# Kernel optimization log

Measured on AMD Instinct MI355X. Metric: run time of the kernel, lower is better.

## Reference

```python
import jax, jax.numpy as jnp
import numpy as np

B, S, D = 16, 4096, 64
N_HASHES = 8
BUCKET_SIZE = 64
N_BUCKETS = S // BUCKET_SIZE  # 64
NEG = -5e4  # the module uses -50000.0 as masking value
EPS = 1e-6


def setup_inputs() -> dict:
    key = jax.random.key(0)
    k1, k2, k3 = jax.random.split(key, 3)
    qk = jax.random.normal(k1, (B, S, D), dtype=jnp.float32)
    v = jax.random.normal(k2, (B, S, D), dtype=jnp.float32)
    # random rotations for LSH: (batch, dim, n_hashes, n_buckets//2)
    rotations = jax.random.normal(k3, (B, D, N_HASHES, N_BUCKETS // 2), dtype=jnp.float32)
    return {"qk": qk, "v": v, "rotations": rotations, "seed_": 0}


def _look_one_back(x):
    # prepend previous chunk (with wraparound) along the key axis
    x_extra = jnp.concatenate([x[:, -1:], x[:, :-1]], axis=1)
    return jnp.concatenate([x, x_extra], axis=2)


def reference(qk, v, rotations, seed_):
    b, s, d = qk.shape
    n_hashes = rotations.shape[2]
    n_buckets = 2 * rotations.shape[3]
    chunks = n_hashes * n_buckets  # n_bins == n_buckets

    # ---- hash_vectors ----
    rot = jnp.einsum('btf,bfhi->bhti', qk, rotations)          # (b, h, s, nb/2)
    rot = jnp.concatenate([rot, -rot], axis=-1)                # (b, h, s, nb)
    buckets = jnp.argmax(rot, axis=-1)                         # (b, h, s)
    offsets = (jnp.arange(n_hashes) * n_buckets)[None, :, None]
    buckets = (buckets + offsets).reshape(b, n_hashes * s)     # (b, h*s)

    # ---- sort by (bucket, position) ----
    ticker = jnp.arange(n_hashes * s)
    buckets_and_t = s * buckets + (ticker % s)[None, :]
    sticker = jnp.argsort(buckets_and_t, axis=-1)              # stable sort indices
    undo_sort = jnp.argsort(sticker, axis=-1)

    st = sticker % s                                           # original positions
    sqk = jnp.take_along_axis(qk, st[..., None], axis=1)       # (b, h*s, d)
    sv = jnp.take_along_axis(v, st[..., None], axis=1)

    bq_t = st.reshape(b, chunks, -1)                           # (b, chunks, bucket)
    bqk = sqk.reshape(b, chunks, -1, d)
    bv = sv.reshape(b, chunks, -1, d)

    bq = bqk
    norm = jnp.linalg.norm(bqk, axis=-1, keepdims=True)
    bk = bqk / (norm + EPS)                                    # make_unit_length

    bk = _look_one_back(bk)                                    # (b, chunks, 2*bucket, d)
    bv = _look_one_back(bv)
    bkv_t = _look_one_back(bq_t[..., None])[..., 0]            # (b, chunks, 2*bucket)

    dots = jnp.einsum('bhie,bhje->bhij', bq, bk) * (d ** -0.5)
    self_mask = bq_t[:, :, :, None] == bkv_t[:, :, None, :]
    dots = jnp.where(self_mask, NEG, dots)

    dots_lse = jax.nn.logsumexp(dots, axis=-1, keepdims=True)  # (b, chunks, bucket, 1)
    probs = jnp.exp(dots - dots_lse)
    bo = jnp.einsum('buij,buje->buie', probs, bv)              # (b, chunks, bucket, d)

    so = bo.reshape(b, n_hashes * s, d)
    slogits = dots_lse.reshape(b, n_hashes * s)

    # ---- unsort ----
    o = jnp.take_along_axis(so, undo_sort[..., None], axis=1)
    logits = jnp.take_along_axis(slogits, undo_sort, axis=-1)

    # ---- combine hash rounds via logsumexp weights ----
    o = o.reshape(b, n_hashes, s, d)
    logits = logits.reshape(b, n_hashes, s, 1)
    w = jnp.exp(logits - jax.nn.logsumexp(logits, axis=1, keepdims=True))
    out = jnp.sum(o * w, axis=1)                               # (b, s, d)
    return out, buckets
```

## Files before the change

### kernel.cpp

```cpp
#include <hip/hip_runtime.h>
#include <math.h>

#define BB   16
#define SS   4096
#define DD   64
#define HH   8
#define NBH  32
#define NB   64
#define NCH  512

typedef __attribute__((ext_vector_type(8))) short s16x8;
typedef __attribute__((ext_vector_type(4))) short s16x4;
typedef __attribute__((ext_vector_type(4))) float f32x4;

static __device__ __forceinline__ unsigned short f2bf(float x) {
  union { float f; unsigned u; } a; a.f = x;
  unsigned r = a.u + 0x7fffu + ((a.u >> 16) & 1u);
  return (unsigned short)(r >> 16);
}
static __device__ __forceinline__ float bf2f(unsigned short u) {
  union { unsigned u; float f; } a; a.u = ((unsigned)u) << 16;
  return a.f;
}

__global__ __launch_bounds__(256) void k_conv(
    const float* __restrict__ qk, const float* __restrict__ v,
    unsigned short* __restrict__ qb, unsigned short* __restrict__ kb,
    unsigned short* __restrict__ vb) {
  const int gid = blockIdx.x * 256 + threadIdx.x;
  const int half = BB * SS * 4;
  const bool isV = gid >= half;
  const int id = isV ? gid - half : gid;
  const int row = id >> 2, q4 = id & 3;

  const float4* src =
      (const float4*)((isV ? v : qk) + (size_t)row * DD + q4 * 16);
  float vals[16];
#pragma unroll
  for (int g = 0; g < 4; g++) {
    const float4 a = src[g];
    vals[g * 4 + 0] = a.x; vals[g * 4 + 1] = a.y;
    vals[g * 4 + 2] = a.z; vals[g * 4 + 3] = a.w;
  }

  if (!isV) {
    float ss = 0.f;
#pragma unroll
    for (int i = 0; i < 16; i++) ss += vals[i] * vals[i];
    ss += __shfl_xor(ss, 1);
    ss += __shfl_xor(ss, 2);
    const float scl = 0.125f / (sqrtf(ss) + 1e-6f);
    unsigned short qo[16], ko[16];
#pragma unroll
    for (int i = 0; i < 16; i++) {
      qo[i] = f2bf(vals[i]);
      ko[i] = f2bf(vals[i] * scl);
    }
    unsigned short* qd = qb + (size_t)row * DD + q4 * 16;
    unsigned short* kd = kb + (size_t)row * DD + q4 * 16;
    *(s16x8*)qd = *(const s16x8*)&qo[0];
    *(s16x8*)(qd + 8) = *(const s16x8*)&qo[8];
    *(s16x8*)kd = *(const s16x8*)&ko[0];
    *(s16x8*)(kd + 8) = *(const s16x8*)&ko[8];
  } else {
    unsigned short vo[16];
#pragma unroll
    for (int i = 0; i < 16; i++) vo[i] = f2bf(vals[i]);
    unsigned short* vd = vb + (size_t)row * DD + q4 * 16;
    *(s16x8*)vd = *(const s16x8*)&vo[0];
    *(s16x8*)(vd + 8) = *(const s16x8*)&vo[8];
  }
}

__global__ __launch_bounds__(256) void k_rotT(
    const float* __restrict__ rot, unsigned short* __restrict__ rTh,
    unsigned short* __restrict__ rTl, int* __restrict__ needy_count) {
  __shared__ float slab[32][256];
  const int b = blockIdx.x;
  const int tid = threadIdx.x;
  if (b == 0 && tid == 0) *needy_count = 0;

  for (int st = 0; st < 2; st++) {
#pragma unroll
    for (int fr = 0; fr < 32; fr++)
      slab[fr][tid] = rot[(size_t)b * (DD * HH * NBH) +
                          (size_t)(st * 32 + fr) * 256 + tid];
    __syncthreads();
    unsigned short hi[32], lo[32];
#pragma unroll
    for (int fr = 0; fr < 32; fr++) {
      const float x = slab[fr][tid];
      const unsigned short hh = f2bf(x);
      hi[fr] = hh;
      lo[fr] = f2bf(x - bf2f(hh));
    }
    unsigned short* dh = rTh + ((size_t)b * 256 + tid) * DD + st * 32;
    unsigned short* dl = rTl + ((size_t)b * 256 + tid) * DD + st * 32;
#pragma unroll
    for (int g = 0; g < 4; g++) {
      *(s16x8*)(dh + g * 8) = *(const s16x8*)&hi[g * 8];
      *(s16x8*)(dl + g * 8) = *(const s16x8*)&lo[g * 8];
    }
    __syncthreads();
  }
}

#define MARGIN 1e-2f

__global__ __launch_bounds__(256, 2) void k_hash_mfma(
    const float* __restrict__ qk, const unsigned short* __restrict__ rTh,
    const unsigned short* __restrict__ rTl, int* __restrict__ bucket_local,
    float* __restrict__ buckets_out, int* __restrict__ needy_list,
    int* __restrict__ needy_count) {
  __shared__ struct __align__(16) {
    unsigned short ah[128][72];
    unsigned short al[128][72];
    float sc[128][33];
  } sm;
  const int b = blockIdx.x;
  const int t0 = blockIdx.y * 128;
  const int tid = threadIdx.x;
  const int w = tid >> 6, lane = tid & 63;
  const int quad = lane >> 4, l16 = lane & 15;

  {
    const int row = tid >> 1, hf = tid & 1;
    const float4* src =
        (const float4*)(qk + ((size_t)b * SS + t0 + row) * DD + hf * 32);
#pragma unroll
    for (int gg = 0; gg < 4; gg++) {
      const float4 v0 = src[gg * 2], v1 = src[gg * 2 + 1];
      const float a[8] = {v0.x, v0.y, v0.z, v0.w, v1.x, v1.y, v1.z, v1.w};
      unsigned short hi[8], lo[8];
#pragma unroll
      for (int e = 0; e < 8; e++) {
        const unsigned short hh = f2bf(a[e]);
        hi[e] = hh;
        lo[e] = f2bf(a[e] - bf2f(hh));
      }
      *(s16x8*)&sm.ah[row][hf * 32 + gg * 8] = *(const s16x8*)hi;
      *(s16x8*)&sm.al[row][hf * 32 + gg * 8] = *(const s16x8*)lo;
    }
  }
  __syncthreads();

  s16x8 Ah[2][2], Al[2][2];
#pragma unroll
  for (int mtl = 0; mtl < 2; mtl++) {
    const int row = (w * 2 + mtl) * 16 + l16;
#pragma unroll
    for (int ks = 0; ks < 2; ks++) {
      Ah[mtl][ks] = *(const s16x8*)&sm.ah[row][ks * 32 + quad * 8];
      Al[mtl][ks] = *(const s16x8*)&sm.al[row][ks * 32 + quad * 8];
    }
  }

#pragma unroll 1
  for (int h = 0; h < HH; h++) {
#pragma unroll
    for (int nt = 0; nt < 2; nt++) {
      const size_t rrow = (((size_t)b * HH + h) * 32 + nt * 16 + l16) * DD;
      s16x8 Bh2[2], Bl2[2];
#pragma unroll
      for (int ks = 0; ks < 2; ks++) {
        Bh2[ks] = *(const s16x8*)&rTh[rrow + ks * 32 + quad * 8];
        Bl2[ks] = *(const s16x8*)&rTl[rrow + ks * 32 + quad * 8];
      }
#pragma unroll
      for (int mtl = 0; mtl < 2; mtl++) {
        f32x4 acc = (f32x4){0.f, 0.f, 0.f, 0.f};
#pragma unroll
        for (int ks = 0; ks < 2; ks++) {
          acc = __builtin_amdgcn_mfma_f32_16x16x32_bf16(Al[mtl][ks], Bl2[ks], acc, 0, 0, 0);
          acc = __builtin_amdgcn_mfma_f32_16x16x32_bf16(Al[mtl][ks], Bh2[ks], acc, 0, 0, 0);
          acc = __builtin_amdgcn_mfma_f32_16x16x32_bf16(Ah[mtl][ks], Bl2[ks], acc, 0, 0, 0);
          acc = __builtin_amdgcn_mfma_f32_16x16x32_bf16(Ah[mtl][ks], Bh2[ks], acc, 0, 0, 0);
        }
#pragma unroll
        for (int r = 0; r < 4; r++)
          sm.sc[(w * 2 + mtl) * 16 + quad * 4 + r][nt * 16 + l16] = acc[r];
      }
    }
    __syncthreads();

    if (lane < 32) {
      const int tloc = w * 32 + lane;
      float best = -3.0e38f, second = -3.0e38f;
      int bi = 0;
#pragma unroll 8
      for (int i = 0; i < 32; i++) {
        const float vv = sm.sc[tloc][i];
        if (vv > best) { second = best; best = vv; bi = i; }
        else if (vv > second) second = vv;
      }
#pragma unroll 8
      for (int i = 32; i < 64; i++) {
        const float vv = -sm.sc[tloc][i - 32];
        if (vv > best) { second = best; best = vv; bi = i; }
        else if (vv > second) second = vv;
      }
      const int t = t0 + tloc;
      bucket_local[((size_t)b * HH + h) * SS + t] = bi;
      buckets_out[(size_t)b * (HH * SS) + (size_t)h * SS + t] =
          (float)(h * NB + bi);
      if (best - second <= MARGIN) {
        const int slot = atomicAdd(needy_count, 1);
        needy_list[slot] = (((b << 3) | h) << 12) | t;
      }
    }
    __syncthreads();
  }
}

__global__ __launch_bounds__(256) void k_hash_fix(
    const float* __restrict__ qk, const float* __restrict__ rot,
    const int* __restrict__ needy_list, const int* __restrict__ needy_count,
    int* __restrict__ bucket_local, float* __restrict__ buckets_out) {
  const int n = *needy_count;
  const int hw = (blockIdx.x * 256 + (int)threadIdx.x) >> 5;
  const int li = threadIdx.x & 31;
  const int nhw = gridDim.x * 8;

  for (int idx = hw; idx < n; idx += nhw) {
    const int code = needy_list[idx];
    const int t = code & 4095;
    const int bh = code >> 12;
    const int b = bh >> 3, h = bh & 7;

    const float* qrow = qk + ((size_t)b * SS + t) * DD;
    const float* rcol = rot + ((size_t)b * DD * HH + h) * NBH + li;

    double acc = 0.0;
#pragma unroll 8
    for (int f = 0; f < DD; f++)
      acc += (double)qrow[f] * (double)rcol[(size_t)f * (HH * NBH)];

    double bv = acc;
    int bi = li;
    if (-acc > bv) { bv = -acc; bi = li + 32; }
#pragma unroll
    for (int off = 1; off < 32; off <<= 1) {
      const double ov = __shfl_xor(bv, off);
      const int oi = __shfl_xor(bi, off);
      if (ov > bv || (ov == bv && oi < bi)) { bv = ov; bi = oi; }
    }
    if (li == 0) {
      bucket_local[((size_t)b * HH + h) * SS + t] = bi;
      buckets_out[(size_t)b * (HH * SS) + (size_t)h * SS + t] =
          (float)(h * NB + bi);
    }
  }
}

__global__ __launch_bounds__(256) void k_sort(
    const int* __restrict__ bucket_local, int* __restrict__ sort_t,
    int* __restrict__ ipos) {
  __shared__ unsigned short lb[SS];
  __shared__ unsigned char  cnt[NB][256];
  __shared__ unsigned short pfx[NB][256];
  __shared__ int part[NB][4];
  __shared__ int tot[NB];
  __shared__ int base[NB];

  const int bh = blockIdx.x;
  const int tid = threadIdx.x;
  const int* src = bucket_local + (size_t)bh * SS;

  int* czero = (int*)&cnt[0][0];
#pragma unroll
  for (int i = 0; i < 16; i++) czero[tid + i * 256] = 0;
  __syncthreads();

#pragma unroll
  for (int i = 0; i < 16; i++) {
    const int t = tid * 16 + i;
    const int v = src[t];
    lb[t] = (unsigned short)v;
    cnt[v][tid]++;
  }
  __syncthreads();

  {
    const int bk = tid & 63, sg = tid >> 6;
    int s = 0;
#pragma unroll 8
    for (int i = 0; i < 64; i++) s += cnt[bk][sg * 64 + i];
    part[bk][sg] = s;
  }
  __syncthreads();
  if (tid < NB) tot[tid] = part[tid][0] + part[tid][1] + part[tid][2] + part[tid][3];
  __syncthreads();
  if (tid == 0) {
    int r = 0;
    for (int i = 0; i < NB; i++) { base[i] = r; r += tot[i]; }
  }
  __syncthreads();
  {
    const int bk = tid & 63, sg = tid >> 6;
    int run = base[bk];
    for (int s = 0; s < sg; s++) run += part[bk][s];
#pragma unroll 8
    for (int i = 0; i < 64; i++) {
      const int th = sg * 64 + i;
      pfx[bk][th] = (unsigned short)run;
      run += cnt[bk][th];
    }
  }
  __syncthreads();
  int* st = sort_t + (size_t)bh * SS;
  int* ip = ipos + (size_t)bh * SS;
#pragma unroll
  for (int i = 0; i < 16; i++) {
    const int t = tid * 16 + i;
    const int bk = lb[t];
    const int pos = pfx[bk][tid]++;
    st[pos] = t;
    ip[t] = pos;
  }
}

__global__ __launch_bounds__(256, 4) void k_attn2(
    const unsigned short* __restrict__ qb, const unsigned short* __restrict__ kbg,
    const unsigned short* __restrict__ vbg, const int* __restrict__ sort_t,
    unsigned short* __restrict__ so, float* __restrict__ lse_u) {
  const int blk = blockIdx.x;
  const int b = blk >> 9;
  const int c = blk & 511;
  const int h = c >> 6, cc = c & 63;
  const int cp = (c + 511) & 511;
  const int hp = cp >> 6, ccp = cp & 63;

  __shared__ struct __align__(16) {
    union {
      unsigned short kb[128][72];
      unsigned short p[64][136];
    } kp;
    unsigned short vs[128][68];
    int tk[128];
  } sm;

  const int tid = threadIdx.x;
  const int w = tid >> 6;
  const int lane = tid & 63;
  const int quad = lane >> 4;
  const int l16 = lane & 15;

  if (tid < 128) {
    const size_t srci = (tid < 64)
        ? (((size_t)b * HH + h) * SS + cc * 64 + tid)
        : (((size_t)b * HH + hp) * SS + ccp * 64 + (tid - 64));
    sm.tk[tid] = sort_t[srci];
  }
  __syncthreads();

  {
    const int j = tid >> 1, hf = tid & 1;
    const int trow = sm.tk[j];
    const s16x8* ksrc = (const s16x8*)(kbg + ((size_t)b * SS + trow) * DD + hf * 32);
    const s16x8* vsrc = (const s16x8*)(vbg + ((size_t)b * SS + trow) * DD + hf * 32);
    s16x8 kr[4], vr[4];
#pragma unroll
    for (int g = 0; g < 4; g++) { kr[g] = ksrc[g]; vr[g] = vsrc[g]; }
#pragma unroll
    for (int g = 0; g < 4; g++)
      *(s16x8*)&sm.kp.kb[j][hf * 32 + g * 8] = kr[g];
#pragma unroll
    for (int g = 0; g < 4; g++) {
      *(s16x4*)&sm.vs[j][hf * 32 + g * 8] = (s16x4){vr[g][0], vr[g][1], vr[g][2], vr[g][3]};
      *(s16x4*)&sm.vs[j][hf * 32 + g * 8 + 4] = (s16x4){vr[g][4], vr[g][5], vr[g][6], vr[g][7]};
    }
  }
  const int tq_frag = sm.tk[w * 16 + l16];
  const unsigned short* qrowp = qb + ((size_t)b * SS + tq_frag) * DD;
  const s16x8 a0 = *(const s16x8*)(qrowp + quad * 8);
  const s16x8 a1 = *(const s16x8*)(qrowp + 32 + quad * 8);
  __syncthreads();

  f32x4 acc[8];
#pragma unroll
  for (int nt = 0; nt < 8; nt++) acc[nt] = (f32x4){0.f, 0.f, 0.f, 0.f};
#pragma unroll
  for (int nt = 0; nt < 8; nt++) {
    const s16x8 b0 = *(const s16x8*)&sm.kp.kb[nt * 16 + l16][quad * 8];
    const s16x8 b1 = *(const s16x8*)&sm.kp.kb[nt * 16 + l16][32 + quad * 8];
    acc[nt] = __builtin_amdgcn_mfma_f32_16x16x32_bf16(a0, b0, acc[nt], 0, 0, 0);
    acc[nt] = __builtin_amdgcn_mfma_f32_16x16x32_bf16(a1, b1, acc[nt], 0, 0, 0);
  }

  int tqr[4];
#pragma unroll
  for (int r = 0; r < 4; r++) tqr[r] = sm.tk[w * 16 + quad * 4 + r];
  int tkc[8];
#pragma unroll
  for (int nt = 0; nt < 8; nt++) tkc[nt] = sm.tk[nt * 16 + l16];

#pragma unroll
  for (int nt = 0; nt < 8; nt++)
#pragma unroll
    for (int r = 0; r < 4; r++)
      if (tqr[r] == tkc[nt]) acc[nt][r] = -50000.0f;

  float rmax[4], lse[4], inv[4];
#pragma unroll
  for (int r = 0; r < 4; r++) {
    float m = acc[0][r];
#pragma unroll
    for (int nt = 1; nt < 8; nt++) m = fmaxf(m, acc[nt][r]);
    m = fmaxf(m, __shfl_xor(m, 1));
    m = fmaxf(m, __shfl_xor(m, 2));
    m = fmaxf(m, __shfl_xor(m, 4));
    m = fmaxf(m, __shfl_xor(m, 8));
    rmax[r] = m;
  }
#pragma unroll
  for (int r = 0; r < 4; r++) {
    float s = 0.f;
#pragma unroll
    for (int nt = 0; nt < 8; nt++) {
      const float e = __expf(acc[nt][r] - rmax[r]);
      acc[nt][r] = e;
      s += e;
    }
    s += __shfl_xor(s, 1);
    s += __shfl_xor(s, 2);
    s += __shfl_xor(s, 4);
    s += __shfl_xor(s, 8);
    inv[r] = 1.0f / s;
    lse[r] = __logf(s) + rmax[r];
  }

  if (l16 == 0) {
#pragma unroll
    for (int r = 0; r < 4; r++)
      lse_u[((size_t)b * SS + tqr[r]) * HH + h] = lse[r];
  }

  __syncthreads();

#pragma unroll
  for (int nt = 0; nt < 8; nt++)
#pragma unroll
    for (int r = 0; r < 4; r++)
      sm.kp.p[w * 16 + quad * 4 + r][nt * 16 + l16] = f2bf(acc[nt][r] * inv[r]);
  __syncthreads();

  f32x4 o[4];
#pragma unroll
  for (int nt = 0; nt < 4; nt++) o[nt] = (f32x4){0.f, 0.f, 0.f, 0.f};
#pragma unroll
  for (int kc = 0; kc < 4; kc++) {
    s16x8 av;
#pragma unroll
    for (int e = 0; e < 8; e++)
      av[e] = (short)sm.vs[kc * 32 + quad * 8 + e][w * 16 + l16];
#pragma unroll
    for (int nt = 0; nt < 4; nt++) {
      const s16x8 bp = *(const s16x8*)&sm.kp.p[nt * 16 + l16][kc * 32 + quad * 8];
      o[nt] = __builtin_amdgcn_mfma_f32_16x16x32_bf16(av, bp, o[nt], 0, 0, 0);
    }
  }

#pragma unroll
  for (int nt = 0; nt < 4; nt++) {
    const int t = sm.tk[nt * 16 + l16];
    s16x4 ov;
#pragma unroll
    for (int r = 0; r < 4; r++) ov[r] = (short)f2bf(o[nt][r]);
    unsigned short* dst =
        so + (((size_t)b * SS + t) * HH + h) * DD + w * 16 + quad * 4;
    *(s16x4*)dst = ov;
  }
}

__global__ __launch_bounds__(256) void k_combine2(
    const unsigned short* __restrict__ so, const float* __restrict__ lse_u,
    float* __restrict__ out) {
  const size_t idx = (size_t)blockIdx.x * 256 + threadIdx.x;
  const int f = (int)(idx & 63);
  const size_t bt = idx >> 6;

  float l[HH];
#pragma unroll
  for (int h = 0; h < HH; h++) l[h] = lse_u[bt * HH + h];
  float m = l[0];
#pragma unroll
  for (int h = 1; h < HH; h++) m = fmaxf(m, l[h]);
  float den = 0.f, num = 0.f;
#pragma unroll
  for (int h = 0; h < HH; h++) {
    const float wgt = __expf(l[h] - m);
    den += wgt;
    num += wgt * bf2f(so[(bt * HH + h) * DD + f]);
  }
  out[idx] = num / den;
}

__global__ __launch_bounds__(256, 2) void k_hash_f32(
    const float* __restrict__ qk, const float* __restrict__ rot,
    int* __restrict__ bucket_local, float* __restrict__ buckets_out,
    int* __restrict__ needy_list, int* __restrict__ needy_count) {
  __shared__ float lb[128 * 65];
  const int b = blockIdx.x;
  const int t0 = blockIdx.y * 128;
  const int tid = threadIdx.x;

  {
    const int row = tid >> 1, hf = (tid & 1) * 32;
    const float4* src =
        (const float4*)(qk + ((size_t)b * SS + t0 + row) * DD + hf);
    float* dst = &lb[row * 65 + hf];
#pragma unroll
    for (int g = 0; g < 8; g++) {
      const float4 vv = src[g];
      dst[g * 4 + 0] = vv.x; dst[g * 4 + 1] = vv.y;
      dst[g * 4 + 2] = vv.z; dst[g * 4 + 3] = vv.w;
    }
  }
  __syncthreads();

  const int w = tid >> 6;
  const int l = tid & 63;
  const int hb = __builtin_amdgcn_readfirstlane(w);

  for (int hp = 0; hp < 2; hp++) {
    const int h = hb + hp * 4;
    const float* rbase = rot + ((size_t)b * DD * HH + h) * NBH;
    const size_t rstride = HH * NBH;

    float acc0[NBH], acc1[NBH];
#pragma unroll
    for (int i = 0; i < NBH; i++) { acc0[i] = 0.f; acc1[i] = 0.f; }

    float4 bufA[8], bufB[8];
#pragma unroll
    for (int i4 = 0; i4 < 8; i4++) bufA[i4] = ((const float4*)rbase)[i4];

    for (int f = 0; f < DD; f += 2) {
      {
        const float4* r4 = (const float4*)(rbase + (size_t)(f + 1) * rstride);
#pragma unroll
        for (int i4 = 0; i4 < 8; i4++) bufB[i4] = r4[i4];
      }
      {
        const float q0 = lb[l * 65 + f];
        const float q1 = lb[(l + 64) * 65 + f];
#pragma unroll
        for (int i4 = 0; i4 < 8; i4++) {
          const float4 rv = bufA[i4];
          acc0[i4*4+0] = fmaf(q0, rv.x, acc0[i4*4+0]);
          acc0[i4*4+1] = fmaf(q0, rv.y, acc0[i4*4+1]);
          acc0[i4*4+2] = fmaf(q0, rv.z, acc0[i4*4+2]);
          acc0[i4*4+3] = fmaf(q0, rv.w, acc0[i4*4+3]);
          acc1[i4*4+0] = fmaf(q1, rv.x, acc1[i4*4+0]);
          acc1[i4*4+1] = fmaf(q1, rv.y, acc1[i4*4+1]);
          acc1[i4*4+2] = fmaf(q1, rv.z, acc1[i4*4+2]);
          acc1[i4*4+3] = fmaf(q1, rv.w, acc1[i4*4+3]);
        }
      }
      if (f + 2 < DD) {
        const float4* r4 = (const float4*)(rbase + (size_t)(f + 2) * rstride);
#pragma unroll
        for (int i4 = 0; i4 < 8; i4++) bufA[i4] = r4[i4];
      }
      {
        const float q0 = lb[l * 65 + f + 1];
        const float q1 = lb[(l + 64) * 65 + f + 1];
#pragma unroll
        for (int i4 = 0; i4 < 8; i4++) {
          const float4 rv = bufB[i4];
          acc0[i4*4+0] = fmaf(q0, rv.x, acc0[i4*4+0]);
          acc0[i4*4+1] = fmaf(q0, rv.y, acc0[i4*4+1]);
          acc0[i4*4+2] = fmaf(q0, rv.z, acc0[i4*4+2]);
          acc0[i4*4+3] = fmaf(q0, rv.w, acc0[i4*4+3]);
          acc1[i4*4+0] = fmaf(q1, rv.x, acc1[i4*4+0]);
          acc1[i4*4+1] = fmaf(q1, rv.y, acc1[i4*4+1]);
          acc1[i4*4+2] = fmaf(q1, rv.z, acc1[i4*4+2]);
          acc1[i4*4+3] = fmaf(q1, rv.w, acc1[i4*4+3]);
        }
      }
    }

#pragma unroll
    for (int tok = 0; tok < 2; tok++) {
      const float* acc = tok ? acc1 : acc0;
      float best = -3.0e38f, second = -3.0e38f;
      int bi = 0;
#pragma unroll
      for (int i = 0; i < 64; i++) {
        const float vv = (i < NBH) ? acc[i] : -acc[i - NBH];
        if (vv > best) { second = best; best = vv; bi = i; }
        else if (vv > second) { second = vv; }
      }
      const int t = t0 + tok * 64 + l;
      bucket_local[((size_t)b * HH + h) * SS + t] = bi;
      buckets_out[(size_t)b * (HH * SS) + (size_t)h * SS + t] =
          (float)(h * NB + bi);
      if (best - second <= MARGIN) {
        const int slot = atomicAdd(needy_count, 1);
        needy_list[slot] = (((b << 3) | h) << 12) | t;
      }
    }
  }
}

__global__ __launch_bounds__(256) void k_attn_atomic(
    const float* __restrict__ qk, const float* __restrict__ v,
    const int* __restrict__ sort_t, float* __restrict__ num,
    float* __restrict__ den) {
  const int blk = blockIdx.x;
  const int b = blk >> 9;
  const int c = blk & 511;
  const int h = c >> 6, cc = c & 63;
  const int cp = (c + 511) & 511;
  const int hp = cp >> 6, ccp = cp & 63;

  __shared__ union {
    struct {
      float qt[DD * 64];
      float kt[DD * 128];
      int   tq[64];
      int   tk[128];
      float nrm[128];
      float red[16 * 64];
      float rmax[64];
      float rsum[64];
    } a;
    struct {
      float pt[128 * 64];
      float vs[128 * 64];
    } p;
  } sm;

  const int tid = threadIdx.x;

  if (tid < 64)
    sm.a.tq[tid] = sort_t[((size_t)b * HH + h) * SS + cc * 64 + tid];
  if (tid >= 128) {
    const int j = tid - 128;
    const size_t src = (j < 64) ? (((size_t)b * HH + h) * SS + cc * 64 + j)
                                : (((size_t)b * HH + hp) * SS + ccp * 64 + (j - 64));
    sm.a.tk[j] = sort_t[src];
  }
  if (tid >= 64 && tid < 192) sm.a.nrm[tid - 64] = 0.f;
  __syncthreads();

  {
    const int qi = tid >> 2, qq = tid & 3;
    const float4* qsrc =
        (const float4*)(qk + ((size_t)b * SS + sm.a.tq[qi]) * DD) + qq * 4;
#pragma unroll
    for (int k4 = 0; k4 < 4; k4++) {
      float4 val = qsrc[k4];
      const int f = qq * 16 + k4 * 4;
      sm.a.qt[(f + 0) * 64 + qi] = val.x;
      sm.a.qt[(f + 1) * 64 + qi] = val.y;
      sm.a.qt[(f + 2) * 64 + qi] = val.z;
      sm.a.qt[(f + 3) * 64 + qi] = val.w;
    }
    const int j = tid >> 1, hhf = tid & 1;
    const float4* ksrc =
        (const float4*)(qk + ((size_t)b * SS + sm.a.tk[j]) * DD) + hhf * 8;
    float ss = 0.f;
#pragma unroll
    for (int k4 = 0; k4 < 8; k4++) {
      float4 val = ksrc[k4];
      const int f = hhf * 32 + k4 * 4;
      sm.a.kt[(f + 0) * 128 + j] = val.x;
      sm.a.kt[(f + 1) * 128 + j] = val.y;
      sm.a.kt[(f + 2) * 128 + j] = val.z;
      sm.a.kt[(f + 3) * 128 + j] = val.w;
      ss += val.x * val.x + val.y * val.y + val.z * val.z + val.w * val.w;
    }
    atomicAdd(&sm.a.nrm[j], ss);
  }
  __syncthreads();
  if (tid < 128) {
    const float n = sqrtf(sm.a.nrm[tid]) + 1e-6f;
    sm.a.nrm[tid] = 0.125f / n;
  }
  float4 vreg[8];
  {
    const int j = tid >> 1, hhf = tid & 1;
    const float4* vsrc =
        (const float4*)(v + ((size_t)b * SS + sm.a.tk[j]) * DD) + hhf * 8;
#pragma unroll
    for (int k4 = 0; k4 < 8; k4++) vreg[k4] = vsrc[k4];
  }
  __syncthreads();

  const int qi0 = (tid & 15) * 4;
  const int j0g = (tid >> 4) * 8;
  const int kg = tid >> 4;
  float acc[4][8];
#pragma unroll
  for (int i = 0; i < 4; i++)
#pragma unroll
    for (int j = 0; j < 8; j++) acc[i][j] = 0.f;

#pragma unroll 8
  for (int f = 0; f < DD; f++) {
    float4 qv = *(const float4*)&sm.a.qt[f * 64 + qi0];
    float4 k0 = *(const float4*)&sm.a.kt[f * 128 + j0g];
    float4 k1 = *(const float4*)&sm.a.kt[f * 128 + j0g + 4];
    float qa[4] = {qv.x, qv.y, qv.z, qv.w};
    float ka[8] = {k0.x, k0.y, k0.z, k0.w, k1.x, k1.y, k1.z, k1.w};
#pragma unroll
    for (int i = 0; i < 4; i++)
#pragma unroll
      for (int j = 0; j < 8; j++) acc[i][j] = fmaf(qa[i], ka[j], acc[i][j]);
  }

  int tqr[4];
#pragma unroll
  for (int i = 0; i < 4; i++) tqr[i] = sm.a.tq[qi0 + i];
  int tkr[8]; float scl[8];
#pragma unroll
  for (int j = 0; j < 8; j++) {
    tkr[j] = sm.a.tk[j0g + j];
    scl[j] = sm.a.nrm[j0g + j];
  }
#pragma unroll
  for (int i = 0; i < 4; i++)
#pragma unroll
    for (int j = 0; j < 8; j++) {
      const float dv = acc[i][j] * scl[j];
      acc[i][j] = (tqr[i] == tkr[j]) ? -50000.0f : dv;
    }

  float pmax[4];
#pragma unroll
  for (int i = 0; i < 4; i++) {
    float m = acc[i][0];
#pragma unroll
    for (int j = 1; j < 8; j++) m = fmaxf(m, acc[i][j]);
    pmax[i] = m;
  }
#pragma unroll
  for (int i = 0; i < 4; i++) sm.a.red[kg * 64 + qi0 + i] = pmax[i];
  __syncthreads();
  if (tid < 64) {
    float m = -3.0e38f;
#pragma unroll
    for (int g = 0; g < 16; g++) m = fmaxf(m, sm.a.red[g * 64 + tid]);
    sm.a.rmax[tid] = m;
  }
  __syncthreads();
  float psum[4];
#pragma unroll
  for (int i = 0; i < 4; i++) {
    const float rm = sm.a.rmax[qi0 + i];
    float s = 0.f;
#pragma unroll
    for (int j = 0; j < 8; j++) {
      const float e = __expf(acc[i][j] - rm);
      acc[i][j] = e;
      s += e;
    }
    psum[i] = s;
  }
#pragma unroll
  for (int i = 0; i < 4; i++) sm.a.red[kg * 64 + qi0 + i] = psum[i];
  __syncthreads();
  if (tid < 64) {
    float s = 0.f;
#pragma unroll
    for (int g = 0; g < 16; g++) s += sm.a.red[g * 64 + tid];
    sm.a.rsum[tid] = s;
  }
  __syncthreads();
  float lse[4], isum[4];
#pragma unroll
  for (int i = 0; i < 4; i++) {
    const float rm = sm.a.rmax[qi0 + i];
    const float s = sm.a.rsum[qi0 + i];
    isum[i] = 1.0f / s;
    lse[i] = __logf(s) + rm;
  }
  __syncthreads();

#pragma unroll
  for (int j = 0; j < 8; j++)
#pragma unroll
    for (int i = 0; i < 4; i++)
      sm.p.pt[(j0g + j) * 64 + qi0 + i] = acc[i][j] * isum[i];
  {
    const int j = tid >> 1, hhf = tid & 1;
#pragma unroll
    for (int k4 = 0; k4 < 8; k4++)
      *(float4*)&sm.p.vs[j * 64 + hhf * 32 + k4 * 4] = vreg[k4];
  }
  __syncthreads();

  const int f0 = (tid >> 4) * 4;
  float o[4][4];
#pragma unroll
  for (int i = 0; i < 4; i++)
#pragma unroll
    for (int j = 0; j < 4; j++) o[i][j] = 0.f;

#pragma unroll 8
  for (int j = 0; j < 128; j++) {
    float4 pv = *(const float4*)&sm.p.pt[j * 64 + qi0];
    float4 vv = *(const float4*)&sm.p.vs[j * 64 + f0];
    float pa[4] = {pv.x, pv.y, pv.z, pv.w};
    float va[4] = {vv.x, vv.y, vv.z, vv.w};
#pragma unroll
    for (int i = 0; i < 4; i++)
#pragma unroll
      for (int j2 = 0; j2 < 4; j2++) o[i][j2] = fmaf(pa[i], va[j2], o[i][j2]);
  }

#pragma unroll
  for (int i = 0; i < 4; i++) {
    const float w = __expf(lse[i]);
    float* dst = num + ((size_t)b * SS + tqr[i]) * DD + f0;
#pragma unroll
    for (int j = 0; j < 4; j++) atomicAdd(dst + j, o[i][j] * w);
    if (kg == 0) atomicAdd(den + (size_t)b * SS + tqr[i], w);
  }
}

__global__ __launch_bounds__(256) void k_final(float* __restrict__ o,
                                               const float* __restrict__ den) {
  const size_t i = (size_t)blockIdx.x * 256 + threadIdx.x;
  o[i] = o[i] / den[i >> 6];
}

extern "C" void kernel_launch(void* const* d_in, const int* in_sizes, int n_in,
                              void* d_out, int out_size, void* d_ws,
                              size_t ws_size, hipStream_t stream) {
  const float* qk  = (const float*)d_in[0];
  const float* v   = (const float*)d_in[1];
  const float* rot = (const float*)d_in[2];

  float* out_attn = (float*)d_out;
  float* buckets_out = out_attn + (size_t)BB * SS * DD;

  const size_t BHS = (size_t)BB * HH * SS;
  const size_t BSD = (size_t)BB * SS * DD;
  const size_t RT  = (size_t)BB * HH * 32 * DD;
  int* bucket_local = (int*)d_ws;
  int* sort_t = bucket_local + BHS;
  int* ipos = sort_t + BHS;
  float* lse_u = (float*)(ipos + BHS);
  unsigned short* qb16 = (unsigned short*)(lse_u + BHS);
  unsigned short* kb16 = qb16 + BSD;
  unsigned short* vb16 = kb16 + BSD;
  unsigned short* so_u = vb16 + BSD;
  unsigned short* rTh = so_u + BHS * DD;
  unsigned short* rTl = rTh + RT;

  const size_t NEED2 =
      4 * BHS * 4 + 3 * BSD * 2 + BHS * DD * 2 + 2 * RT * 2;

  if (ws_size >= NEED2) {
    k_conv<<<2 * BB * SS * 4 / 256, 256, 0, stream>>>(qk, v, qb16, kb16, vb16);
    k_rotT<<<BB, 256, 0, stream>>>(rot, rTh, rTl, ipos);
    k_hash_mfma<<<dim3(BB, SS / 128), 256, 0, stream>>>(
        qk, rTh, rTl, bucket_local, buckets_out, sort_t, ipos);
    k_hash_fix<<<256, 256, 0, stream>>>(qk, rot, sort_t, ipos, bucket_local,
                                        buckets_out);
    k_sort<<<BB * HH, 256, 0, stream>>>(bucket_local, sort_t, ipos);
    k_attn2<<<BB * NCH, 256, 0, stream>>>(qb16, kb16, vb16, sort_t, so_u, lse_u);
    k_combine2<<<(BB * SS * DD) / 256, 256, 0, stream>>>(so_u, lse_u, out_attn);
  } else {
    float* den = (float*)(sort_t + 2 * BHS);
    hipMemsetAsync(out_attn, 0, (size_t)BB * SS * DD * sizeof(float), stream);
    hipMemsetAsync(den, 0, (size_t)BB * SS * sizeof(float), stream);
    hipMemsetAsync(ipos, 0, sizeof(int), stream);
    k_hash_f32<<<dim3(BB, SS / 128), 256, 0, stream>>>(
        qk, rot, bucket_local, buckets_out, sort_t, ipos);
    k_hash_fix<<<256, 256, 0, stream>>>(qk, rot, sort_t, ipos, bucket_local,
                                        buckets_out);
    k_sort<<<BB * HH, 256, 0, stream>>>(bucket_local, sort_t, ipos);
    k_attn_atomic<<<BB * NCH, 256, 0, stream>>>(qk, v, sort_t, out_attn, den);
    k_final<<<(BB * SS * DD) / 256, 256, 0, stream>>>(out_attn, den);
  }
}
```

Before: 236.5 us.

## Transpose V in LDS, simplify self-mask, and split argmax across half-waves

```diff
diff --git a/kernel.cpp b/kernel.cpp
--- a/kernel.cpp
+++ b/kernel.cpp
@@ -183,29 +183,35 @@
     }
     __syncthreads();
 
-    if (lane < 32) {
-      const int tloc = w * 32 + lane;
+    {
+      const int l32 = lane & 31;
+      const int tloc = w * 32 + l32;
+      const bool neg = lane >= 32;
+      const float sgn = neg ? -1.0f : 1.0f;
       float best = -3.0e38f, second = -3.0e38f;
       int bi = 0;
 #pragma unroll 8
       for (int i = 0; i < 32; i++) {
-        const float vv = sm.sc[tloc][i];
+        const float vv = sgn * sm.sc[tloc][i];
         if (vv > best) { second = best; best = vv; bi = i; }
         else if (vv > second) second = vv;
       }
-#pragma unroll 8
-      for (int i = 32; i < 64; i++) {
-        const float vv = -sm.sc[tloc][i - 32];
-        if (vv > best) { second = best; best = vv; bi = i; }
-        else if (vv > second) second = vv;
-      }
-      const int t = t0 + tloc;
-      bucket_local[((size_t)b * HH + h) * SS + t] = bi;
-      buckets_out[(size_t)b * (HH * SS) + (size_t)h * SS + t] =
-          (float)(h * NB + bi);
-      if (best - second <= MARGIN) {
-        const int slot = atomicAdd(needy_count, 1);
-        needy_list[slot] = (((b << 3) | h) << 12) | t;
+      if (neg) bi += 32;
+      const float ob = __shfl_xor(best, 32);
+      const float os = __shfl_xor(second, 32);
+      const int obi = __shfl_xor(bi, 32);
+      if (lane < 32) {
+        const float ms = fmaxf(fminf(best, ob), fmaxf(second, os));
+        float mb = best; int mbi = bi;
+        if (ob > best) { mb = ob; mbi = obi; }
+        const int t = t0 + tloc;
+        bucket_local[((size_t)b * HH + h) * SS + t] = mbi;
+        buckets_out[(size_t)b * (HH * SS) + (size_t)h * SS + t] =
+            (float)(h * NB + mbi);
+        if (mb - ms <= MARGIN) {
+          const int slot = atomicAdd(needy_count, 1);
+          needy_list[slot] = (((b << 3) | h) << 12) | t;
+        }
       }
     }
     __syncthreads();
@@ -335,7 +341,7 @@
       unsigned short kb[128][72];
       unsigned short p[64][136];
     } kp;
-    unsigned short vs[128][68];
+    unsigned short vsT[64][136];
     int tk[128];
   } sm;
 
@@ -357,17 +363,29 @@
     const int j = tid >> 1, hf = tid & 1;
     const int trow = sm.tk[j];
     const s16x8* ksrc = (const s16x8*)(kbg + ((size_t)b * SS + trow) * DD + hf * 32);
-    const s16x8* vsrc = (const s16x8*)(vbg + ((size_t)b * SS + trow) * DD + hf * 32);
-    s16x8 kr[4], vr[4];
-#pragma unroll
-    for (int g = 0; g < 4; g++) { kr[g] = ksrc[g]; vr[g] = vsrc[g]; }
+    s16x8 kr[4];
+#pragma unroll
+    for (int g = 0; g < 4; g++) kr[g] = ksrc[g];
 #pragma unroll
     for (int g = 0; g < 4; g++)
       *(s16x8*)&sm.kp.kb[j][hf * 32 + g * 8] = kr[g];
-#pragma unroll
-    for (int g = 0; g < 4; g++) {
-      *(s16x4*)&sm.vs[j][hf * 32 + g * 8] = (s16x4){vr[g][0], vr[g][1], vr[g][2], vr[g][3]};
-      *(s16x4*)&sm.vs[j][hf * 32 + g * 8 + 4] = (s16x4){vr[g][4], vr[g][5], vr[g][6], vr[g][7]};
+  }
+  {
+    const int fg = tid >> 5;
+    const int tg = (tid & 31) << 2;
+    const unsigned short* vb_b = vbg + (size_t)b * SS * DD + fg * 8;
+    const s16x8 vr0 = *(const s16x8*)(vb_b + (size_t)sm.tk[tg + 0] * DD);
+    const s16x8 vr1 = *(const s16x8*)(vb_b + (size_t)sm.tk[tg + 1] * DD);
+    const s16x8 vr2 = *(const s16x8*)(vb_b + (size_t)sm.tk[tg + 2] * DD);
+    const s16x8 vr3 = *(const s16x8*)(vb_b + (size_t)sm.tk[tg + 3] * DD);
+#pragma unroll
+    for (int i = 0; i < 8; i++) {
+      uint2 val;
+      val.x = ((unsigned)(unsigned short)vr0[i]) |
+              (((unsigned)(unsigned short)vr1[i]) << 16);
+      val.y = ((unsigned)(unsigned short)vr2[i]) |
+              (((unsigned)(unsigned short)vr3[i]) << 16);
+      *(uint2*)&sm.vsT[fg * 8 + i][tg] = val;
     }
   }
   const int tq_frag = sm.tk[w * 16 + l16];
@@ -390,15 +408,24 @@
   int tqr[4];
 #pragma unroll
   for (int r = 0; r < 4; r++) tqr[r] = sm.tk[w * 16 + quad * 4 + r];
-  int tkc[8];
-#pragma unroll
-  for (int nt = 0; nt < 8; nt++) tkc[nt] = sm.tk[nt * 16 + l16];
-
-#pragma unroll
-  for (int nt = 0; nt < 8; nt++)
-#pragma unroll
-    for (int r = 0; r < 4; r++)
-      if (tqr[r] == tkc[nt]) acc[nt][r] = -50000.0f;
+
+#pragma unroll
+  for (int nt = 0; nt < 4; nt++) {
+    if (nt == w) {
+#pragma unroll
+      for (int r = 0; r < 4; r++)
+        if (l16 == quad * 4 + r) acc[nt][r] = -50000.0f;
+    }
+  }
+  if (cc == 0) {
+#pragma unroll
+    for (int nt = 4; nt < 8; nt++) {
+      const int tkcv = sm.tk[nt * 16 + l16];
+#pragma unroll
+      for (int r = 0; r < 4; r++)
+        if (tqr[r] == tkcv) acc[nt][r] = -50000.0f;
+    }
+  }
 
   float rmax[4], lse[4], inv[4];
 #pragma unroll
@@ -447,12 +474,10 @@
   f32x4 o[4];
 #pragma unroll
   for (int nt = 0; nt < 4; nt++) o[nt] = (f32x4){0.f, 0.f, 0.f, 0.f};
+  const unsigned short* vrow = &sm.vsT[w * 16 + l16][0];
 #pragma unroll
   for (int kc = 0; kc < 4; kc++) {
-    s16x8 av;
-#pragma unroll
-    for (int e = 0; e < 8; e++)
-      av[e] = (short)sm.vs[kc * 32 + quad * 8 + e][w * 16 + l16];
+    const s16x8 av = *(const s16x8*)(vrow + kc * 32 + quad * 8);
 #pragma unroll
     for (int nt = 0; nt < 4; nt++) {
       const s16x8 bp = *(const s16x8*)&sm.kp.p[nt * 16 + l16][kc * 32 + quad * 8];
```

After: 221.1 us. 6.5% less time.
